# Performance work log

Hardware: AMD Instinct MI355X
Metric: run time of the kernel (lower is better)

Reference implementation:

```python
import jax, jax.numpy as jnp
import numpy as np

INF = 100000000.0
TOPK = 13
ALPHA = 1
BETA = 6


def box_cxcywh_to_xyxy(b):
    cx, cy, w, h = jnp.split(b, 4, axis=-1)
    return jnp.concatenate([cx - 0.5 * w, cy - 0.5 * h, cx + 0.5 * w, cy + 0.5 * h], axis=-1)


def generalized_box_iou(boxes1, boxes2):
    # boxes1: [N,4] xyxy, boxes2: [G,4] xyxy -> [N,G]
    area1 = (boxes1[:, 2] - boxes1[:, 0]) * (boxes1[:, 3] - boxes1[:, 1])
    area2 = (boxes2[:, 2] - boxes2[:, 0]) * (boxes2[:, 3] - boxes2[:, 1])
    lt = jnp.maximum(boxes1[:, None, :2], boxes2[None, :, :2])
    rb = jnp.minimum(boxes1[:, None, 2:], boxes2[None, :, 2:])
    wh = jnp.clip(rb - lt, 0.0)
    inter = wh[..., 0] * wh[..., 1]
    union = area1[:, None] + area2[None, :] - inter
    iou = inter / union
    lt_e = jnp.minimum(boxes1[:, None, :2], boxes2[None, :, :2])
    rb_e = jnp.maximum(boxes1[:, None, 2:], boxes2[None, :, 2:])
    wh_e = jnp.clip(rb_e - lt_e, 0.0)
    area_e = wh_e[..., 0] * wh_e[..., 1]
    return iou - (area_e - union) / area_e


def _assign_one(cls_logits, bbox_pred, gt_boxes, gt_labels):
    # cls_logits [N,C], bbox_pred [N,4] cxcywh, gt_boxes [G,4] cxcywh, gt_labels [G]
    N = bbox_pred.shape[0]
    G = gt_boxes.shape[0]
    scores = jax.nn.sigmoid(cls_logits)
    overlaps = -generalized_box_iou(box_cxcywh_to_xyxy(bbox_pred), box_cxcywh_to_xyxy(gt_boxes))  # [N,G]
    bbox_scores = scores[:, gt_labels]                       # [N,G] gather per-gt class score
    alignment = bbox_scores ** ALPHA * overlaps ** BETA      # [N,G]
    # per-gt topk over queries
    cand_metrics, cand_idxs = jax.lax.top_k(alignment.T, TOPK)  # [G,K]
    is_pos = cand_metrics > 0
    vals = jnp.take_along_axis(overlaps.T, cand_idxs, axis=1)   # [G,K]
    rows = jnp.broadcast_to(jnp.arange(G)[:, None], (G, TOPK))
    cols = jnp.where(is_pos, cand_idxs, N)  # out-of-bounds col -> dropped
    oinf = jnp.full((G, N), -INF, dtype=overlaps.dtype)
    oinf = oinf.at[rows, cols].set(vals, mode='drop')
    max_overlaps = oinf.max(axis=0)     # [N]
    argmax_overlaps = oinf.argmax(axis=0)
    pos = max_overlaps != -INF
    assigned_gt_inds = jnp.where(pos, argmax_overlaps + 1, 0)
    assign_metrics = jnp.where(pos, alignment[jnp.arange(N), argmax_overlaps], 0.0)
    assigned_labels = jnp.where(pos, gt_labels[argmax_overlaps], -1)
    return assigned_gt_inds, assigned_labels, assign_metrics


def setup_inputs() -> dict:
    key = jax.random.key(0)
    k1, k2, k3, k4 = jax.random.split(key, 4)
    bs, N, C, G = 16, 4000, 80, 300
    return {
        'pred_logits': jax.random.normal(k1, (bs, N, C), dtype=jnp.float32),
        'pred_boxes': jax.random.uniform(k2, (bs, N, 4), dtype=jnp.float32, minval=0.05, maxval=0.95),
        'gt_boxes': jax.random.uniform(k3, (bs, G, 4), dtype=jnp.float32, minval=0.05, maxval=0.95),
        'gt_labels': jax.random.randint(k4, (bs, G), 0, C),
    }


def reference(pred_logits, pred_boxes, gt_boxes, gt_labels):
    # Fixed-shape equivalent of matched_list: assigned_gt_inds[b,q] == 0 means
    # background; k>0 means query q matched to gt k-1 (same semantics as the
    # (valid_query_idx, valid_assigned_gt_inds) pairs in the torch code).
    return jax.vmap(_assign_one)(pred_logits, pred_boxes, gt_boxes, gt_labels)
```

## Files before the change

### kernel.cpp

```cpp
#include <hip/hip_runtime.h>

#define NPRED  4000
#define NGROUP 1000
#define NGT    300
#define NCLS   80
#define TOPKK  13
#define NCHUNK 125

typedef unsigned long long u64;

__device__ __forceinline__ float frcp(float x) { return __builtin_amdgcn_rcpf(x); }
__device__ __forceinline__ float fexp(float x) {
    return __builtin_amdgcn_exp2f(x * 1.44269504088896341f);
}

__device__ __forceinline__ float neg_giou_x(float4 p, float gx1, float gy1,
                                            float gx2, float gy2, float garea) {
    float pa  = (p.z - p.x) * (p.w - p.y);
    float whx = fmaxf(fminf(p.z, gx2) - fmaxf(p.x, gx1), 0.0f);
    float why = fmaxf(fminf(p.w, gy2) - fmaxf(p.y, gy1), 0.0f);
    float inter = whx * why;
    float uni = pa + garea - inter;
    float iou = inter * frcp(uni);
    float wex = fmaxf(p.z, gx2) - fminf(p.x, gx1);
    float wey = fmaxf(p.w, gy2) - fminf(p.y, gy1);
    float area_e = wex * wey;
    return (area_e - uni) * frcp(area_e) - iou;
}

__device__ __forceinline__ float4 to_xyxy(float4 pb) {
    return make_float4(pb.x - 0.5f * pb.z, pb.y - 0.5f * pb.w,
                       pb.x + 0.5f * pb.z, pb.y + 0.5f * pb.w);
}

__device__ __forceinline__ float sigmoid_fast(float x) {
    return frcp(1.0f + fexp(-x));
}

__device__ __forceinline__ float pow6(float x) {
    float x2 = x * x;
    float x4 = x2 * x2;
    return x2 * x4;
}

__device__ __forceinline__ unsigned ord_float(float f) {
    unsigned u = __float_as_uint(f);
    return u ^ ((unsigned)(((int)u) >> 31) | 0x80000000u);
}

__device__ __forceinline__ u64 pack_key(float v, int n) {
    return ((u64)__float_as_uint(v) << 32) | (u64)(~(unsigned)n);
}

__global__ void init_keys(u64* keys, int n) {
    int i = blockIdx.x * blockDim.x + threadIdx.x;
    if (i < n) keys[i] = 0ULL;
}

__global__ __launch_bounds__(256) void sig_transpose(const float* __restrict__ logits,
                                                     const float4* __restrict__ pboxes,
                                                     float* __restrict__ st,
                                                     float4* __restrict__ pxyxy,
                                                     u64* __restrict__ keys,
                                                     int total_keys) {
    const int tid = threadIdx.x;
    const int gid = blockIdx.x * 256 + tid;
    if (gid < total_keys) keys[gid] = 0ULL;

    const int b = blockIdx.x / NCHUNK;
    const int n0 = (blockIdx.x % NCHUNK) * 32;

    if (tid < 32) {
        pxyxy[(size_t)b * NPRED + n0 + tid] =
            to_xyxy(pboxes[(size_t)b * NPRED + n0 + tid]);
    }

    __shared__ float tile[NCLS][32 + 1];

    const float4* src = (const float4*)(logits + ((size_t)b * NPRED + n0) * NCLS);
    #pragma unroll
    for (int it = 0; it < 3; ++it) {
        int i4 = tid + it * 256;
        if (i4 < 640) {
            int p = i4 / 20;
            int c = (i4 - p * 20) * 4;
            float4 v = src[i4];
            tile[c + 0][p] = sigmoid_fast(v.x);
            tile[c + 1][p] = sigmoid_fast(v.y);
            tile[c + 2][p] = sigmoid_fast(v.z);
            tile[c + 3][p] = sigmoid_fast(v.w);
        }
    }
    __syncthreads();
    float* dstbase = st + (size_t)b * NCLS * NPRED + n0;
    #pragma unroll
    for (int it = 0; it < 3; ++it) {
        int w4 = tid + it * 256;
        if (w4 < 640) {
            int c = w4 >> 3, r4 = (w4 & 7) * 4;
            float4 v = make_float4(tile[c][r4], tile[c][r4 + 1],
                                   tile[c][r4 + 2], tile[c][r4 + 3]);
            *(float4*)(dstbase + (size_t)c * NPRED + r4) = v;
        }
    }
}

template <bool PRE>
__global__ __launch_bounds__(256) void topk_scatter(const float* __restrict__ logits,
                                                    const float* __restrict__ st,
                                                    const float4* __restrict__ pboxes,
                                                    const float4* __restrict__ pxyxy,
                                                    const float4* __restrict__ gboxes,
                                                    const int* __restrict__ glabels,
                                                    u64* __restrict__ keys) {
    const int blk = blockIdx.x;
    const int b = blk / NGT;
    const int g = blk - b * NGT;
    const int tid = threadIdx.x;
    const int wave = tid >> 6;
    const int lane = tid & 63;

    __shared__ __align__(16) float s_key[NPRED];
    __shared__ u64 s_wave[4];
    __shared__ u64 s_win[TOPKK];

    float4 gb = gboxes[b * NGT + g];
    const int lab = glabels[b * NGT + g];
    const float gx1 = gb.x - 0.5f * gb.z;
    const float gy1 = gb.y - 0.5f * gb.w;
    const float gx2 = gb.x + 0.5f * gb.z;
    const float gy2 = gb.y + 0.5f * gb.w;
    const float garea = (gx2 - gx1) * (gy2 - gy1);

    const float* lg = logits + (size_t)b * NPRED * NCLS + lab;
    const float* srow = st + ((size_t)b * NCLS + lab) * NPRED;
    const float4* srow4 = (const float4*)srow;
    const float4* pbb = pboxes + (size_t)b * NPRED;
    const float4* pxr = pxyxy + (size_t)b * NPRED;

    u64 b1 = 0ULL, b2 = 0ULL;
    #pragma unroll
    for (int j = 0; j < 4; ++j) {
        int grp = tid + j * 256;
        if (grp < NGROUP) {
            int n0 = grp * 4;
            float s0, s1, s2, s3;
            float4 p0, p1, p2, p3;
            if (PRE) {
                float4 s4 = srow4[grp];
                s0 = s4.x; s1 = s4.y; s2 = s4.z; s3 = s4.w;
                p0 = pxr[n0]; p1 = pxr[n0 + 1]; p2 = pxr[n0 + 2]; p3 = pxr[n0 + 3];
            } else {
                s0 = sigmoid_fast(lg[(size_t)(n0 + 0) * NCLS]);
                s1 = sigmoid_fast(lg[(size_t)(n0 + 1) * NCLS]);
                s2 = sigmoid_fast(lg[(size_t)(n0 + 2) * NCLS]);
                s3 = sigmoid_fast(lg[(size_t)(n0 + 3) * NCLS]);
                p0 = to_xyxy(pbb[n0]);     p1 = to_xyxy(pbb[n0 + 1]);
                p2 = to_xyxy(pbb[n0 + 2]); p3 = to_xyxy(pbb[n0 + 3]);
            }
            float v0 = s0 * pow6(neg_giou_x(p0, gx1, gy1, gx2, gy2, garea));
            float v1 = s1 * pow6(neg_giou_x(p1, gx1, gy1, gx2, gy2, garea));
            float v2 = s2 * pow6(neg_giou_x(p2, gx1, gy1, gx2, gy2, garea));
            float v3 = s3 * pow6(neg_giou_x(p3, gx1, gy1, gx2, gy2, garea));
            *(float4*)&s_key[n0] = make_float4(v0, v1, v2, v3);
            u64 k0 = pack_key(v0, n0);
            u64 k1 = pack_key(v1, n0 + 1);
            u64 k2 = pack_key(v2, n0 + 2);
            u64 k3 = pack_key(v3, n0 + 3);
            if (k0 > b1) { b2 = b1; b1 = k0; } else if (k0 > b2) b2 = k0;
            if (k1 > b1) { b2 = b1; b1 = k1; } else if (k1 > b2) b2 = k1;
            if (k2 > b1) { b2 = b1; b1 = k2; } else if (k2 > b2) b2 = k2;
            if (k3 > b1) { b2 = b1; b1 = k3; } else if (k3 > b2) b2 = k3;
        }
    }

    {
        u64 m1 = b1;
        #pragma unroll
        for (int m = 1; m < 64; m <<= 1) {
            u64 o = __shfl_xor(m1, m, 64);
            if (o > m1) m1 = o;
        }
        if (lane == 0) s_wave[wave] = m1;
    }

    int nwin = 0;
    for (int k = 0; k < TOPKK; ++k) {
        __syncthreads();
        u64 t1 = s_wave[0];
        u64 c;
        c = s_wave[1]; if (c > t1) t1 = c;
        c = s_wave[2]; if (c > t1) t1 = c;
        c = s_wave[3]; if (c > t1) t1 = c;
        if ((unsigned)(t1 >> 32) == 0u) break;
        if (tid == 0) s_win[k] = t1;
        nwin = k + 1;
        int n1 = (int)(~(unsigned)t1);
        int ownerTid = (n1 >> 2) & 255;
        if (tid == ownerTid) {
            s_key[n1] = 0.0f;
            if (b2 != 0ULL) { b1 = b2; b2 = 0ULL; }
            else {
                b1 = 0ULL;
                #pragma unroll
                for (int jj = 0; jj < 4; ++jj) {
                    int grp = tid + jj * 256;
                    if (grp >= NGROUP) continue;
                    int n0 = grp * 4;
                    float4 q = *(const float4*)&s_key[n0];
                    u64 c0 = pack_key(q.x, n0);
                    u64 c1 = pack_key(q.y, n0 + 1);
                    u64 c2 = pack_key(q.z, n0 + 2);
                    u64 c3 = pack_key(q.w, n0 + 3);
                    if (c0 > b1) { b2 = b1; b1 = c0; } else if (c0 > b2) b2 = c0;
                    if (c1 > b1) { b2 = b1; b1 = c1; } else if (c1 > b2) b2 = c1;
                    if (c2 > b1) { b2 = b1; b1 = c2; } else if (c2 > b2) b2 = c2;
                    if (c3 > b1) { b2 = b1; b1 = c3; } else if (c3 > b2) b2 = c3;
                }
            }
        }
        if ((ownerTid >> 6) == wave) {
            u64 m1 = b1;
            #pragma unroll
            for (int m = 1; m < 64; m <<= 1) {
                u64 o = __shfl_xor(m1, m, 64);
                if (o > m1) m1 = o;
            }
            if (lane == 0) s_wave[wave] = m1;
        }
    }
    __syncthreads();

    if (tid < nwin) {
        u64 t = s_win[tid];
        int wi = (int)(~(unsigned)t);
        float o;
        if (PRE) {
            o = neg_giou_x(pxr[wi], gx1, gy1, gx2, gy2, garea);
        } else {
            o = neg_giou_x(to_xyxy(pbb[wi]), gx1, gy1, gx2, gy2, garea);
        }
        unsigned mbits = (unsigned)(t >> 32) >> 16;
        u64 key = ((u64)ord_float(o) << 32)
                | ((u64)(511u - (unsigned)g) << 23)
                | ((u64)mbits << 7);
        atomicMax(&keys[(size_t)b * NPRED + wi], key);
    }
}

__global__ void finalize(const int* __restrict__ glabels,
                         const u64* __restrict__ keys,
                         float* __restrict__ out, int total) {
    int i = blockIdx.x * blockDim.x + threadIdx.x;
    if (i >= total) return;
    int b = i / NPRED;
    u64 key = keys[i];
    float o0 = 0.0f, o1 = -1.0f, o2 = 0.0f;
    if (key != 0ULL) {
        int g = 511 - (int)((key >> 23) & 0x1FF);
        o0 = (float)(g + 1);
        o1 = (float)glabels[b * NGT + g];
        o2 = __uint_as_float(((unsigned)(key >> 7) & 0xFFFFu) << 16);
    }
    out[i] = o0;
    out[(size_t)total + i] = o1;
    out[(size_t)2 * total + i] = o2;
}

extern "C" void kernel_launch(void* const* d_in, const int* in_sizes, int n_in,
                              void* d_out, int out_size, void* d_ws, size_t ws_size,
                              hipStream_t stream) {
    const float* logits  = (const float*)d_in[0];
    const float4* pboxes = (const float4*)d_in[1];
    const float4* gboxes = (const float4*)d_in[2];
    const int* glabels   = (const int*)d_in[3];

    const int bs = in_sizes[3] / NGT;
    const int total = bs * NPRED;
    char* ws = (char*)d_ws;
    u64* keys   = (u64*)ws;                    ws += (size_t)total * 8;
    float* st   = (float*)ws;                  ws += (size_t)bs * NCLS * NPRED * 4;
    float4* pxy = (float4*)ws;                 ws += (size_t)total * 16;
    float* out = (float*)d_out;

    const size_t need = (size_t)(ws - (char*)d_ws);
    if (ws_size >= need) {
        sig_transpose<<<bs * NCHUNK, 256, 0, stream>>>(logits, pboxes, st, pxy,
                                                       keys, total);
        topk_scatter<true><<<bs * NGT, 256, 0, stream>>>(logits, st, pboxes, pxy,
                                                         gboxes, glabels, keys);
    } else {
        init_keys<<<(total + 255) / 256, 256, 0, stream>>>(keys, total);
        topk_scatter<false><<<bs * NGT, 256, 0, stream>>>(logits, st, pboxes, pxy,
                                                          gboxes, glabels, keys);
    }
    finalize<<<(total + 255) / 256, 256, 0, stream>>>(glabels, keys, out, total);
}
```

Before: 123.4 us.

## Process two ground-truth boxes per block with 512 threads, sharing box loads

The top-k scatter kernel now handles two ground-truth boxes per block with 512 threads. Each predicted box load is reused for both GTs, and the two 13-round top-k selections share each round's barrier, roughly halving block count and sync rounds per GT. In exchange it doubles shared memory per block, adds register pressure for two running top-2 states, and raises the owner thread's serial rescan work per round.

```diff
diff --git a/kernel.cpp b/kernel.cpp
--- a/kernel.cpp
+++ b/kernel.cpp
@@ -3,8 +3,9 @@
 #define NPRED  4000
 #define NGROUP 1000
 #define NGT    300
+#define NGTH   150
+#define TOPKK  13
 #define NCLS   80
-#define TOPKK  13
 #define NCHUNK 125
 
 typedef unsigned long long u64;
@@ -52,6 +53,10 @@
     return ((u64)__float_as_uint(v) << 32) | (u64)(~(unsigned)n);
 }
 
+__device__ __forceinline__ void top2_upd(u64& b1, u64& b2, u64 k) {
+    if (k > b1) { b2 = b1; b1 = k; } else if (k > b2) b2 = k;
+}
+
 __global__ void init_keys(u64* keys, int n) {
     int i = blockIdx.x * blockDim.x + threadIdx.x;
     if (i < n) keys[i] = 0ULL;
@@ -106,7 +111,7 @@
 }
 
 template <bool PRE>
-__global__ __launch_bounds__(256) void topk_scatter(const float* __restrict__ logits,
+__global__ __launch_bounds__(512) void topk_scatter(const float* __restrict__ logits,
                                                     const float* __restrict__ st,
                                                     const float4* __restrict__ pboxes,
                                                     const float4* __restrict__ pxyxy,
@@ -114,132 +119,203 @@
                                                     const int* __restrict__ glabels,
                                                     u64* __restrict__ keys) {
     const int blk = blockIdx.x;
-    const int b = blk / NGT;
-    const int g = blk - b * NGT;
+    const int b = blk / NGTH;
+    const int g0 = (blk - b * NGTH) * 2;
     const int tid = threadIdx.x;
     const int wave = tid >> 6;
     const int lane = tid & 63;
 
-    __shared__ __align__(16) float s_key[NPRED];
-    __shared__ u64 s_wave[4];
-    __shared__ u64 s_win[TOPKK];
-
-    float4 gb = gboxes[b * NGT + g];
-    const int lab = glabels[b * NGT + g];
-    const float gx1 = gb.x - 0.5f * gb.z;
-    const float gy1 = gb.y - 0.5f * gb.w;
-    const float gx2 = gb.x + 0.5f * gb.z;
-    const float gy2 = gb.y + 0.5f * gb.w;
-    const float garea = (gx2 - gx1) * (gy2 - gy1);
-
-    const float* lg = logits + (size_t)b * NPRED * NCLS + lab;
-    const float* srow = st + ((size_t)b * NCLS + lab) * NPRED;
-    const float4* srow4 = (const float4*)srow;
+    __shared__ __align__(16) float s_key0[NPRED];
+    __shared__ __align__(16) float s_key1[NPRED];
+    __shared__ __align__(16) u64 s_wave[2][8];
+    __shared__ u64 s_win[2][TOPKK];
+
+    float4 gbA = gboxes[b * NGT + g0];
+    float4 gbB = gboxes[b * NGT + g0 + 1];
+    const int labA = glabels[b * NGT + g0];
+    const int labB = glabels[b * NGT + g0 + 1];
+    const float ax1 = gbA.x - 0.5f * gbA.z, ay1 = gbA.y - 0.5f * gbA.w;
+    const float ax2 = gbA.x + 0.5f * gbA.z, ay2 = gbA.y + 0.5f * gbA.w;
+    const float aga = (ax2 - ax1) * (ay2 - ay1);
+    const float bx1 = gbB.x - 0.5f * gbB.z, by1 = gbB.y - 0.5f * gbB.w;
+    const float bx2 = gbB.x + 0.5f * gbB.z, by2 = gbB.y + 0.5f * gbB.w;
+    const float bga = (bx2 - bx1) * (by2 - by1);
+
+    const float* lgA = logits + (size_t)b * NPRED * NCLS + labA;
+    const float* lgB = logits + (size_t)b * NPRED * NCLS + labB;
+    const float4* srowA4 = (const float4*)(st + ((size_t)b * NCLS + labA) * NPRED);
+    const float4* srowB4 = (const float4*)(st + ((size_t)b * NCLS + labB) * NPRED);
     const float4* pbb = pboxes + (size_t)b * NPRED;
     const float4* pxr = pxyxy + (size_t)b * NPRED;
 
-    u64 b1 = 0ULL, b2 = 0ULL;
+    u64 a1 = 0ULL, a2 = 0ULL;
+    u64 c1 = 0ULL, c2 = 0ULL;
     #pragma unroll
-    for (int j = 0; j < 4; ++j) {
-        int grp = tid + j * 256;
+    for (int j = 0; j < 2; ++j) {
+        int grp = tid + j * 512;
         if (grp < NGROUP) {
             int n0 = grp * 4;
-            float s0, s1, s2, s3;
-            float4 p0, p1, p2, p3;
+            float4 sA, sB, p0, p1, p2, p3;
             if (PRE) {
-                float4 s4 = srow4[grp];
-                s0 = s4.x; s1 = s4.y; s2 = s4.z; s3 = s4.w;
+                sA = srowA4[grp]; sB = srowB4[grp];
                 p0 = pxr[n0]; p1 = pxr[n0 + 1]; p2 = pxr[n0 + 2]; p3 = pxr[n0 + 3];
             } else {
-                s0 = sigmoid_fast(lg[(size_t)(n0 + 0) * NCLS]);
-                s1 = sigmoid_fast(lg[(size_t)(n0 + 1) * NCLS]);
-                s2 = sigmoid_fast(lg[(size_t)(n0 + 2) * NCLS]);
-                s3 = sigmoid_fast(lg[(size_t)(n0 + 3) * NCLS]);
+                sA = make_float4(sigmoid_fast(lgA[(size_t)(n0 + 0) * NCLS]),
+                                 sigmoid_fast(lgA[(size_t)(n0 + 1) * NCLS]),
+                                 sigmoid_fast(lgA[(size_t)(n0 + 2) * NCLS]),
+                                 sigmoid_fast(lgA[(size_t)(n0 + 3) * NCLS]));
+                sB = make_float4(sigmoid_fast(lgB[(size_t)(n0 + 0) * NCLS]),
+                                 sigmoid_fast(lgB[(size_t)(n0 + 1) * NCLS]),
+                                 sigmoid_fast(lgB[(size_t)(n0 + 2) * NCLS]),
+                                 sigmoid_fast(lgB[(size_t)(n0 + 3) * NCLS]));
                 p0 = to_xyxy(pbb[n0]);     p1 = to_xyxy(pbb[n0 + 1]);
                 p2 = to_xyxy(pbb[n0 + 2]); p3 = to_xyxy(pbb[n0 + 3]);
             }
-            float v0 = s0 * pow6(neg_giou_x(p0, gx1, gy1, gx2, gy2, garea));
-            float v1 = s1 * pow6(neg_giou_x(p1, gx1, gy1, gx2, gy2, garea));
-            float v2 = s2 * pow6(neg_giou_x(p2, gx1, gy1, gx2, gy2, garea));
-            float v3 = s3 * pow6(neg_giou_x(p3, gx1, gy1, gx2, gy2, garea));
-            *(float4*)&s_key[n0] = make_float4(v0, v1, v2, v3);
-            u64 k0 = pack_key(v0, n0);
-            u64 k1 = pack_key(v1, n0 + 1);
-            u64 k2 = pack_key(v2, n0 + 2);
-            u64 k3 = pack_key(v3, n0 + 3);
-            if (k0 > b1) { b2 = b1; b1 = k0; } else if (k0 > b2) b2 = k0;
-            if (k1 > b1) { b2 = b1; b1 = k1; } else if (k1 > b2) b2 = k1;
-            if (k2 > b1) { b2 = b1; b1 = k2; } else if (k2 > b2) b2 = k2;
-            if (k3 > b1) { b2 = b1; b1 = k3; } else if (k3 > b2) b2 = k3;
+            float vA0 = sA.x * pow6(neg_giou_x(p0, ax1, ay1, ax2, ay2, aga));
+            float vA1 = sA.y * pow6(neg_giou_x(p1, ax1, ay1, ax2, ay2, aga));
+            float vA2 = sA.z * pow6(neg_giou_x(p2, ax1, ay1, ax2, ay2, aga));
+            float vA3 = sA.w * pow6(neg_giou_x(p3, ax1, ay1, ax2, ay2, aga));
+            *(float4*)&s_key0[n0] = make_float4(vA0, vA1, vA2, vA3);
+            top2_upd(a1, a2, pack_key(vA0, n0));
+            top2_upd(a1, a2, pack_key(vA1, n0 + 1));
+            top2_upd(a1, a2, pack_key(vA2, n0 + 2));
+            top2_upd(a1, a2, pack_key(vA3, n0 + 3));
+            float vB0 = sB.x * pow6(neg_giou_x(p0, bx1, by1, bx2, by2, bga));
+            float vB1 = sB.y * pow6(neg_giou_x(p1, bx1, by1, bx2, by2, bga));
+            float vB2 = sB.z * pow6(neg_giou_x(p2, bx1, by1, bx2, by2, bga));
+            float vB3 = sB.w * pow6(neg_giou_x(p3, bx1, by1, bx2, by2, bga));
+            *(float4*)&s_key1[n0] = make_float4(vB0, vB1, vB2, vB3);
+            top2_upd(c1, c2, pack_key(vB0, n0));
+            top2_upd(c1, c2, pack_key(vB1, n0 + 1));
+            top2_upd(c1, c2, pack_key(vB2, n0 + 2));
+            top2_upd(c1, c2, pack_key(vB3, n0 + 3));
         }
     }
 
     {
-        u64 m1 = b1;
+        u64 mA = a1, mB = c1;
         #pragma unroll
         for (int m = 1; m < 64; m <<= 1) {
-            u64 o = __shfl_xor(m1, m, 64);
-            if (o > m1) m1 = o;
-        }
-        if (lane == 0) s_wave[wave] = m1;
-    }
-
-    int nwin = 0;
+            u64 oA = __shfl_xor(mA, m, 64);
+            u64 oB = __shfl_xor(mB, m, 64);
+            if (oA > mA) mA = oA;
+            if (oB > mB) mB = oB;
+        }
+        if (lane == 0) { s_wave[0][wave] = mA; s_wave[1][wave] = mB; }
+    }
+
+    int nwin0 = 0, nwin1 = 0;
+    bool alive0 = true, alive1 = true;
     for (int k = 0; k < TOPKK; ++k) {
         __syncthreads();
-        u64 t1 = s_wave[0];
-        u64 c;
-        c = s_wave[1]; if (c > t1) t1 = c;
-        c = s_wave[2]; if (c > t1) t1 = c;
-        c = s_wave[3]; if (c > t1) t1 = c;
-        if ((unsigned)(t1 >> 32) == 0u) break;
-        if (tid == 0) s_win[k] = t1;
-        nwin = k + 1;
-        int n1 = (int)(~(unsigned)t1);
-        int ownerTid = (n1 >> 2) & 255;
-        if (tid == ownerTid) {
-            s_key[n1] = 0.0f;
-            if (b2 != 0ULL) { b1 = b2; b2 = 0ULL; }
-            else {
-                b1 = 0ULL;
+        u64 t0 = 0ULL, t1 = 0ULL;
+        if (alive0) {
+            const ulonglong2* sw = (const ulonglong2*)&s_wave[0][0];
+            ulonglong2 q0 = sw[0], q1 = sw[1], q2 = sw[2], q3 = sw[3];
+            t0 = q0.x;
+            if (q0.y > t0) t0 = q0.y;
+            if (q1.x > t0) t0 = q1.x;
+            if (q1.y > t0) t0 = q1.y;
+            if (q2.x > t0) t0 = q2.x;
+            if (q2.y > t0) t0 = q2.y;
+            if (q3.x > t0) t0 = q3.x;
+            if (q3.y > t0) t0 = q3.y;
+            if ((unsigned)(t0 >> 32) == 0u) alive0 = false;
+            else { if (tid == 0) s_win[0][k] = t0; nwin0 = k + 1; }
+        }
+        if (alive1) {
+            const ulonglong2* sw = (const ulonglong2*)&s_wave[1][0];
+            ulonglong2 q0 = sw[0], q1 = sw[1], q2 = sw[2], q3 = sw[3];
+            t1 = q0.x;
+            if (q0.y > t1) t1 = q0.y;
+            if (q1.x > t1) t1 = q1.x;
+            if (q1.y > t1) t1 = q1.y;
+            if (q2.x > t1) t1 = q2.x;
+            if (q2.y > t1) t1 = q2.y;
+            if (q3.x > t1) t1 = q3.x;
+            if (q3.y > t1) t1 = q3.y;
+            if ((unsigned)(t1 >> 32) == 0u) alive1 = false;
+            else { if (tid == 0) s_win[1][k] = t1; nwin1 = k + 1; }
+        }
+        if (!alive0 && !alive1) break;
+        if (alive0) {
+            int n1 = (int)(~(unsigned)t0);
+            int grp = n1 >> 2;
+            int ownerTid = (grp >= 512) ? grp - 512 : grp;
+            if (tid == ownerTid) {
+                s_key0[n1] = 0.0f;
+                if (a2 != 0ULL) { a1 = a2; a2 = 0ULL; }
+                else {
+                    a1 = 0ULL;
+                    #pragma unroll
+                    for (int jj = 0; jj < 2; ++jj) {
+                        int gp = tid + jj * 512;
+                        if (gp >= NGROUP) continue;
+                        int n0 = gp * 4;
+                        float4 q = *(const float4*)&s_key0[n0];
+                        top2_upd(a1, a2, pack_key(q.x, n0));
+                        top2_upd(a1, a2, pack_key(q.y, n0 + 1));
+                        top2_upd(a1, a2, pack_key(q.z, n0 + 2));
+                        top2_upd(a1, a2, pack_key(q.w, n0 + 3));
+                    }
+                }
+            }
+            if ((ownerTid >> 6) == wave) {
+                u64 m1 = a1;
                 #pragma unroll
-                for (int jj = 0; jj < 4; ++jj) {
-                    int grp = tid + jj * 256;
-                    if (grp >= NGROUP) continue;
-                    int n0 = grp * 4;
-                    float4 q = *(const float4*)&s_key[n0];
-                    u64 c0 = pack_key(q.x, n0);
-                    u64 c1 = pack_key(q.y, n0 + 1);
-                    u64 c2 = pack_key(q.z, n0 + 2);
-                    u64 c3 = pack_key(q.w, n0 + 3);
-                    if (c0 > b1) { b2 = b1; b1 = c0; } else if (c0 > b2) b2 = c0;
-                    if (c1 > b1) { b2 = b1; b1 = c1; } else if (c1 > b2) b2 = c1;
-                    if (c2 > b1) { b2 = b1; b1 = c2; } else if (c2 > b2) b2 = c2;
-                    if (c3 > b1) { b2 = b1; b1 = c3; } else if (c3 > b2) b2 = c3;
+                for (int m = 1; m < 64; m <<= 1) {
+                    u64 o = __shfl_xor(m1, m, 64);
+                    if (o > m1) m1 = o;
                 }
-            }
-        }
-        if ((ownerTid >> 6) == wave) {
-            u64 m1 = b1;
-            #pragma unroll
-            for (int m = 1; m < 64; m <<= 1) {
-                u64 o = __shfl_xor(m1, m, 64);
-                if (o > m1) m1 = o;
-            }
-            if (lane == 0) s_wave[wave] = m1;
+                if (lane == 0) s_wave[0][wave] = m1;
+            }
+        }
+        if (alive1) {
+            int n1 = (int)(~(unsigned)t1);
+            int grp = n1 >> 2;
+            int ownerTid = (grp >= 512) ? grp - 512 : grp;
+            if (tid == ownerTid) {
+                s_key1[n1] = 0.0f;
+                if (c2 != 0ULL) { c1 = c2; c2 = 0ULL; }
+                else {
+                    c1 = 0ULL;
+                    #pragma unroll
+                    for (int jj = 0; jj < 2; ++jj) {
+                        int gp = tid + jj * 512;
+                        if (gp >= NGROUP) continue;
+                        int n0 = gp * 4;
+                        float4 q = *(const float4*)&s_key1[n0];
+                        top2_upd(c1, c2, pack_key(q.x, n0));
+                        top2_upd(c1, c2, pack_key(q.y, n0 + 1));
+                        top2_upd(c1, c2, pack_key(q.z, n0 + 2));
+                        top2_upd(c1, c2, pack_key(q.w, n0 + 3));
+                    }
+                }
+            }
+            if ((ownerTid >> 6) == wave) {
+                u64 m1 = c1;
+                #pragma unroll
+                for (int m = 1; m < 64; m <<= 1) {
+                    u64 o = __shfl_xor(m1, m, 64);
+                    if (o > m1) m1 = o;
+                }
+                if (lane == 0) s_wave[1][wave] = m1;
+            }
         }
     }
     __syncthreads();
 
-    if (tid < nwin) {
-        u64 t = s_win[tid];
+    int which = -1, slot = 0;
+    if (tid < nwin0) { which = 0; slot = tid; }
+    else if (tid >= 64 && tid - 64 < nwin1) { which = 1; slot = tid - 64; }
+    if (which >= 0) {
+        u64 t = s_win[which][slot];
         int wi = (int)(~(unsigned)t);
+        int g = g0 + which;
         float o;
-        if (PRE) {
-            o = neg_giou_x(pxr[wi], gx1, gy1, gx2, gy2, garea);
-        } else {
-            o = neg_giou_x(to_xyxy(pbb[wi]), gx1, gy1, gx2, gy2, garea);
-        }
+        float4 p = PRE ? pxr[wi] : to_xyxy(pbb[wi]);
+        if (which == 0) o = neg_giou_x(p, ax1, ay1, ax2, ay2, aga);
+        else            o = neg_giou_x(p, bx1, by1, bx2, by2, bga);
         unsigned mbits = (unsigned)(t >> 32) >> 16;
         u64 key = ((u64)ord_float(o) << 32)
                 | ((u64)(511u - (unsigned)g) << 23)
@@ -287,12 +363,12 @@
     if (ws_size >= need) {
         sig_transpose<<<bs * NCHUNK, 256, 0, stream>>>(logits, pboxes, st, pxy,
                                                        keys, total);
-        topk_scatter<true><<<bs * NGT, 256, 0, stream>>>(logits, st, pboxes, pxy,
-                                                         gboxes, glabels, keys);
+        topk_scatter<true><<<bs * NGTH, 512, 0, stream>>>(logits, st, pboxes, pxy,
+                                                          gboxes, glabels, keys);
     } else {
         init_keys<<<(total + 255) / 256, 256, 0, stream>>>(keys, total);
-        topk_scatter<false><<<bs * NGT, 256, 0, stream>>>(logits, st, pboxes, pxy,
-                                                          gboxes, glabels, keys);
+        topk_scatter<false><<<bs * NGTH, 512, 0, stream>>>(logits, st, pboxes, pxy,
+                                                           gboxes, glabels, keys);
     }
     finalize<<<(total + 255) / 256, 256, 0, stream>>>(glabels, keys, out, total);
 }
```

New measurement: 257.4 us. 109% more time.
